# Optimization experiments

Hardware: AMD Instinct MI355X
Metric: run time of the kernel (lower is better)

The kernel has to match this reference:

```python
import jax, jax.numpy as jnp
import numpy as np

HEAD, SIZE = 16, 64
DIM = HEAD * SIZE
NINF = -10000.0
EPS = 1e-6


def setup_inputs() -> dict:
    key = jax.random.key(0)
    ks = jax.random.split(key, 12)
    B, S = 4, 2048
    std = 0.02
    return {
        "x": jax.random.normal(ks[0], (B, S, DIM), jnp.float32),
        "mask": jax.random.randint(ks[1], (B, S), 0, 2, jnp.int32),
        "wq_w": jax.random.normal(ks[2], (DIM, DIM), jnp.float32) * std,
        "wq_b": jnp.zeros((DIM,), jnp.float32),
        "wk_w": jax.random.normal(ks[3], (DIM, DIM), jnp.float32) * std,
        "wk_b": jnp.zeros((DIM,), jnp.float32),
        "wv_w": jax.random.normal(ks[4], (DIM, DIM), jnp.float32) * std,
        "wv_b": jnp.zeros((DIM,), jnp.float32),
        "dense_w": jax.random.normal(ks[5], (DIM, DIM), jnp.float32) * std,
        "dense_b": jnp.zeros((DIM,), jnp.float32),
        "gamma": jnp.ones((DIM,), jnp.float32),
        "beta": jnp.zeros((DIM,), jnp.float32),
    }


def _split_heads(t):
    # [B, S, DIM] -> [B, H, S, size]
    B, S, _ = t.shape
    return t.reshape(B, S, HEAD, SIZE).transpose(0, 2, 1, 3)


def _layernorm(x, gamma, beta):
    mu = jnp.mean(x, axis=-1, keepdims=True)
    var = jnp.mean(jnp.square(x - mu), axis=-1, keepdims=True)
    return (x - mu) * jax.lax.rsqrt(var + EPS) * gamma + beta


def reference(x, mask, wq_w, wq_b, wk_w, wk_b, wv_w, wv_b, dense_w, dense_b, gamma, beta):
    B, S, _ = x.shape
    q = _split_heads(x @ wq_w + wq_b)
    k = _split_heads(x @ wk_w + wk_b)
    v = _split_heads(x @ wv_w + wv_b)
    # scores [B, H, S, S]
    scores = jnp.einsum("bhqd,bhkd->bhqk", q, k) / jnp.sqrt(jnp.float32(SIZE))
    scores = scores + mask.astype(jnp.float32)[:, None, None, :] * NINF
    attn = jax.nn.softmax(scores, axis=-1)
    ctx = jnp.einsum("bhqk,bhkd->bhqd", attn, v)  # [B, H, S, size]
    ctx = ctx.transpose(0, 2, 1, 3).reshape(B, S, DIM)
    out = _layernorm(x + (ctx @ dense_w + dense_b), gamma, beta)
    return out, attn
```

## Files before the change

### kernel.cpp

```cpp
#include <hip/hip_runtime.h>
#include <stdint.h>

#define NB 4
#define NS 2048
#define NH 16
#define HSZ 64
#define ND 1024
#define NM (NB*NS)
#define QSCALE 0.180336880f

typedef unsigned short u16;
typedef unsigned int u32;
typedef __attribute__((ext_vector_type(4))) float f32x4;
typedef __attribute__((ext_vector_type(8))) __bf16 bf16x8;

static __device__ __forceinline__ u16 f2bf(float f){
  unsigned int x = __builtin_bit_cast(unsigned int, f);
  x += 0x7fffu + ((x >> 16) & 1u);
  return (u16)(x >> 16);
}
static __device__ __forceinline__ u16 f2bf_rz(float f){
  return (u16)(__builtin_bit_cast(unsigned int, f) >> 16);
}

#define GLDS16(gp, lp) __builtin_amdgcn_global_load_lds( \
    (const __attribute__((address_space(1))) void*)(gp),  \
    (__attribute__((address_space(3))) void*)(lp), 16, 0, 0)

__global__ __launch_bounds__(256) void k_cast(const float4* __restrict__ in,
                                              ushort4* __restrict__ out, int n4){
  int i = blockIdx.x*256 + threadIdx.x;
  if (i >= n4) return;
  float4 v = in[i];
  ushort4 o;
  o.x = f2bf(v.x); o.y = f2bf(v.y); o.z = f2bf(v.z); o.w = f2bf(v.w);
  out[i] = o;
}

__global__ __launch_bounds__(256) void k_transpose4(const float* __restrict__ wq,
    const float* __restrict__ wk, const float* __restrict__ wv,
    const float* __restrict__ wd, u16* __restrict__ wcat, u16* __restrict__ wdt){
  __shared__ float t[32][33];
  const int z = blockIdx.z;
  const float* in = (z==0) ? wq : (z==1) ? wk : (z==2) ? wv : wd;
  u16* out = (z<3) ? (wcat + (size_t)z*ND*ND) : wdt;
  int tx = threadIdx.x & 31, ty = threadIdx.x >> 5;
  int n0 = blockIdx.x*32, k0 = blockIdx.y*32;
  #pragma unroll
  for (int i=0;i<32;i+=8)
    t[ty+i][tx] = in[(size_t)(k0+ty+i)*ND + n0 + tx];
  __syncthreads();
  #pragma unroll
  for (int i=0;i<32;i+=8)
    out[(size_t)(n0+ty+i)*ND + k0 + tx] = f2bf(t[tx][ty+i]);
}

template<int EPI>
__global__ __launch_bounds__(256,2) void k_gemm(const u16* __restrict__ A,
    const u16* __restrict__ Bt, const float* __restrict__ b0,
    const float* __restrict__ b1, const float* __restrict__ b2,
    const float* __restrict__ resid, u16* __restrict__ Qo, u16* __restrict__ Ko,
    u16* __restrict__ Vto, float* __restrict__ Out){
  __shared__ u16 sA[128*64];
  __shared__ u16 sB[128*64];
  const int tid = threadIdx.x;
  const int wave = tid >> 6, lane = tid & 63;
  const int l15 = lane & 15, l4 = lane >> 4;
  const int m0 = blockIdx.x * 128, n0 = blockIdx.y * 128;
  const int wm = wave >> 1, wn = wave & 1;
  const f32x4 vz = {0.f,0.f,0.f,0.f};
  f32x4 acc[4][4];
  #pragma unroll
  for (int i=0;i<4;i++)
    #pragma unroll
    for (int j=0;j<4;j++) acc[i][j] = vz;

  for (int k0 = 0; k0 < 1024; k0 += 64){
    __syncthreads();
    #pragma unroll
    for (int t=0; t<4; t++){
      const int jb = (t*4 + wave)*64;
      const int j  = jb + lane;
      const int r = j >> 3, c = (j & 7) << 3;
      GLDS16(A  + (((size_t)(m0 + r)) << 10) + (size_t)(k0 + c), sA + jb*8);
      GLDS16(Bt + (((size_t)(n0 + r)) << 10) + (size_t)(k0 + c), sB + jb*8);
    }
    __syncthreads();
    #pragma unroll
    for (int kk=0; kk<64; kk+=32){
      bf16x8 af[4], bv[4];
      #pragma unroll
      for (int mi=0;mi<4;mi++)
        af[mi] = *(const bf16x8*)(const void*)(sA + (wm*64 + mi*16 + l15)*64 + kk + l4*8);
      #pragma unroll
      for (int ni=0;ni<4;ni++)
        bv[ni] = *(const bf16x8*)(const void*)(sB + (wn*64 + ni*16 + l15)*64 + kk + l4*8);
      #pragma unroll
      for (int mi=0;mi<4;mi++)
        #pragma unroll
        for (int ni=0;ni<4;ni++)
          acc[mi][ni] = __builtin_amdgcn_mfma_f32_16x16x32_bf16(af[mi], bv[ni], acc[mi][ni], 0, 0, 0);
    }
  }

  if (EPI == 0){
    const int sec = n0 >> 10;
    const float* bias = (sec==0) ? b0 : (sec==1) ? b1 : b2;
    const float scale = (sec==0) ? QSCALE : 1.0f;
    u16* dst = (sec==0) ? Qo : (sec==1) ? Ko : Vto;
    #pragma unroll
    for (int mi=0;mi<4;mi++){
      #pragma unroll
      for (int ni=0;ni<4;ni++){
        const int n = n0 + wn*64 + ni*16 + l15;
        const int nn = n & (ND-1);
        const int h = nn >> 6, d = nn & 63;
        const float bvv = bias[nn];
        #pragma unroll
        for (int j=0;j<4;j++){
          const int m = m0 + wm*64 + mi*16 + l4*4 + j;
          const int b = m >> 11, s = m & (NS-1);
          const float v = (acc[mi][ni][j] + bvv) * scale;
          if (sec < 2)
            dst[((((size_t)b*NH + h)*NS + s) << 6) + d] = f2bf(v);
          else
            dst[((((size_t)b*NH + h)*HSZ + d) << 11) + s] = f2bf(v);
        }
      }
    }
  } else {
    #pragma unroll
    for (int mi=0;mi<4;mi++){
      #pragma unroll
      for (int ni=0;ni<4;ni++){
        const int n = n0 + wn*64 + ni*16 + l15;
        const float bvv = b0[n];
        #pragma unroll
        for (int j=0;j<4;j++){
          const int m = m0 + wm*64 + mi*16 + l4*4 + j;
          const size_t o = ((size_t)m << 10) + n;
          Out[o] = acc[mi][ni][j] + bvv + resid[o];
        }
      }
    }
  }
}

static __device__ __forceinline__ void attn_decode(int bid, int& qb, int& bh){
  const int x = bid & 7, t = bid >> 3;
  qb = t & 15;
  bh = (t >> 4) * 8 + x;
}

__global__ __launch_bounds__(512,4) void k_attn_stats(const u16* __restrict__ Q,
    const u16* __restrict__ K, const int* __restrict__ mask,
    float* __restrict__ stats){
  __shared__ u16 sK[64][72];
  const int tid = threadIdx.x, wave = tid>>6, lane = tid&63;
  const int l15 = lane&15, l4 = lane>>4;
  int qb, bh; attn_decode(blockIdx.x, qb, bh);
  const int b = bh >> 4;
  const size_t hoff = (size_t)bh * NS * HSZ;
  const int q0 = qb*128 + wave*16;
  const bf16x8 qf0 = *(const bf16x8*)(const void*)(Q + hoff + (size_t)(q0+l15)*HSZ + l4*8);
  const bf16x8 qf1 = *(const bf16x8*)(const void*)(Q + hoff + (size_t)(q0+l15)*HSZ + 32 + l4*8);
  const f32x4 vz = {0.f,0.f,0.f,0.f};
  float lr[4] = {0.f,0.f,0.f,0.f};
  for (int kb=0; kb<NS; kb+=64){
    __syncthreads();
    {
      const int r = tid >> 3, c = (tid & 7) << 3;
      *(int4*)(void*)&sK[r][c] = *(const int4*)(const void*)(K + hoff + (size_t)(kb+r)*HSZ + c);
    }
    __syncthreads();
    #pragma unroll
    for (int n=0;n<4;n++){
      bf16x8 kf0 = *(const bf16x8*)(const void*)&sK[n*16+l15][l4*8];
      bf16x8 kf1 = *(const bf16x8*)(const void*)&sK[n*16+l15][32+l4*8];
      f32x4 a = vz;
      a = __builtin_amdgcn_mfma_f32_16x16x32_bf16(qf0, kf0, a, 0,0,0);
      a = __builtin_amdgcn_mfma_f32_16x16x32_bf16(qf1, kf1, a, 0,0,0);
      const int key = kb + n*16 + l15;
      const bool msk = mask[b*NS + key] != 0;
      #pragma unroll
      for (int j=0;j<4;j++)
        lr[j] += msk ? 0.f : __builtin_amdgcn_exp2f(a[j]);
    }
  }
  #pragma unroll
  for (int j=0;j<4;j++){
    float l = lr[j];
    #pragma unroll
    for (int off=1; off<16; off<<=1)
      l += __shfl_xor(l, off, 64);
    if (l15 == 0)
      stats[(size_t)bh*NS + q0 + l4*4 + j] = 1.f/l;
  }
}

__global__ __launch_bounds__(512,4) void k_attn_pv(const u16* __restrict__ Q,
    const u16* __restrict__ K, const u16* __restrict__ Vt,
    const int* __restrict__ mask, const float* __restrict__ stats,
    float* __restrict__ attn, u16* __restrict__ ctx){
  __shared__ u16 sK[64][72];
  __shared__ u16 sV[64][72];
  __shared__ u16 sP[8][16][72];
  const int tid = threadIdx.x, wave = tid>>6, lane = tid&63;
  const int l15 = lane&15, l4 = lane>>4;
  int qb, bh; attn_decode(blockIdx.x, qb, bh);
  const int b = bh >> 4, h = bh & 15;
  const size_t hoff = (size_t)bh * NS * HSZ;
  const int q0 = qb*128 + wave*16;
  const bf16x8 qf0 = *(const bf16x8*)(const void*)(Q + hoff + (size_t)(q0+l15)*HSZ + l4*8);
  const bf16x8 qf1 = *(const bf16x8*)(const void*)(Q + hoff + (size_t)(q0+l15)*HSZ + 32 + l4*8);
  float rinv[4];
  #pragma unroll
  for (int j=0;j<4;j++)
    rinv[j] = stats[(size_t)bh*NS + q0 + l4*4 + j];
  const f32x4 vz = {0.f,0.f,0.f,0.f};
  f32x4 cacc[4];
  #pragma unroll
  for (int i=0;i<4;i++) cacc[i] = vz;
  float* attn_base = attn + (size_t)bh * NS * NS;

  for (int kb=0; kb<NS; kb+=64){
    __syncthreads();
    {
      const int r = tid >> 3, c = (tid & 7) << 3;
      *(int4*)(void*)&sK[r][c] = *(const int4*)(const void*)(K  + hoff + (size_t)(kb+r)*HSZ + c);
      *(int4*)(void*)&sV[r][c] = *(const int4*)(const void*)(Vt + hoff + (size_t)r*NS + kb + c);
    }
    __syncthreads();
    #pragma unroll
    for (int n=0;n<4;n++){
      bf16x8 kf0 = *(const bf16x8*)(const void*)&sK[n*16+l15][l4*8];
      bf16x8 kf1 = *(const bf16x8*)(const void*)&sK[n*16+l15][32+l4*8];
      f32x4 a = vz;
      a = __builtin_amdgcn_mfma_f32_16x16x32_bf16(qf0, kf0, a, 0,0,0);
      a = __builtin_amdgcn_mfma_f32_16x16x32_bf16(qf1, kf1, a, 0,0,0);
      const int key = kb + n*16 + l15;
      const bool msk = mask[b*NS + key] != 0;
      #pragma unroll
      for (int j=0;j<4;j++){
        const float e = msk ? 0.f : __builtin_amdgcn_exp2f(a[j]);
        sP[wave][l4*4+j][n*16+l15] = f2bf_rz(e * rinv[j]);
      }
    }
    #pragma unroll
    for (int kk=0;kk<2;kk++){
      bf16x8 pf = *(const bf16x8*)(const void*)&sP[wave][l15][kk*32 + l4*8];
      #pragma unroll
      for (int n2=0;n2<4;n2++){
        bf16x8 vf = *(const bf16x8*)(const void*)&sV[n2*16+l15][kk*32 + l4*8];
        cacc[n2] = __builtin_amdgcn_mfma_f32_16x16x32_bf16(pf, vf, cacc[n2], 0,0,0);
      }
    }
    #pragma unroll
    for (int jj=0;jj<4;jj++){
      const int r = jj*4 + l4;
      const uint2 pw = *(const uint2*)(const void*)&sP[wave][r][l15*4];
      f32x4 o;
      o.x = __builtin_bit_cast(float, pw.x << 16);
      o.y = __builtin_bit_cast(float, pw.x & 0xffff0000u);
      o.z = __builtin_bit_cast(float, pw.y << 16);
      o.w = __builtin_bit_cast(float, pw.y & 0xffff0000u);
      __builtin_nontemporal_store(o,
          (f32x4*)(void*)&attn_base[(size_t)(q0 + r)*NS + kb + l15*4]);
    }
  }
  #pragma unroll
  for (int n2=0;n2<4;n2++)
    #pragma unroll
    for (int j=0;j<4;j++){
      const int q = q0 + l4*4 + j;
      ctx[(((size_t)(b*NS + q)) << 10) + h*HSZ + n2*16 + l15] = f2bf(cacc[n2][j]);
    }
}

__global__ __launch_bounds__(256) void k_layernorm(float* __restrict__ buf,
    const float* __restrict__ gamma, const float* __restrict__ beta){
  const int row = blockIdx.x, tid = threadIdx.x;
  float4* rp = (float4*)(buf + ((size_t)row << 10));
  float4 a = rp[tid];
  float s  = a.x + a.y + a.z + a.w;
  float ss = a.x*a.x + a.y*a.y + a.z*a.z + a.w*a.w;
  #pragma unroll
  for (int off=1; off<64; off<<=1){
    s  += __shfl_xor(s,  off, 64);
    ss += __shfl_xor(ss, off, 64);
  }
  __shared__ float red[8];
  const int wave = tid>>6, lane = tid&63;
  if (lane == 0){ red[wave] = s; red[wave+4] = ss; }
  __syncthreads();
  s  = red[0]+red[1]+red[2]+red[3];
  ss = red[4]+red[5]+red[6]+red[7];
  const float mu  = s * (1.f/1024.f);
  const float var = ss * (1.f/1024.f) - mu*mu;
  const float rs  = rsqrtf(var + 1e-6f);
  float4 g  = ((const float4*)gamma)[tid];
  float4 be = ((const float4*)beta)[tid];
  float4 o;
  o.x = (a.x-mu)*rs*g.x + be.x;
  o.y = (a.y-mu)*rs*g.y + be.y;
  o.z = (a.z-mu)*rs*g.z + be.z;
  o.w = (a.w-mu)*rs*g.w + be.w;
  rp[tid] = o;
}

extern "C" void kernel_launch(void* const* d_in, const int* in_sizes, int n_in,
                              void* d_out, int out_size, void* d_ws, size_t ws_size,
                              hipStream_t stream){
  const float* x     = (const float*)d_in[0];
  const int*   mask  = (const int*)d_in[1];
  const float* wq_w  = (const float*)d_in[2];
  const float* wq_b  = (const float*)d_in[3];
  const float* wk_w  = (const float*)d_in[4];
  const float* wk_b  = (const float*)d_in[5];
  const float* wv_w  = (const float*)d_in[6];
  const float* wv_b  = (const float*)d_in[7];
  const float* wd_w  = (const float*)d_in[8];
  const float* wd_b  = (const float*)d_in[9];
  const float* gamma = (const float*)d_in[10];
  const float* beta  = (const float*)d_in[11];

  float* out0 = (float*)d_out;
  float* attn = out0 + (size_t)NM * ND;

  char* ws = (char*)d_ws;
  u16*   xb    = (u16*)(ws);
  u16*   ctx   = (u16*)(ws);
  u16*   wcat  = (u16*)(ws + (16u<<20));
  u16*   wdt   = (u16*)(ws + (22u<<20));
  u16*   Qb    = (u16*)(ws + (24u<<20));
  u16*   Kb    = (u16*)(ws + (40u<<20));
  u16*   Vtb   = (u16*)(ws + (56u<<20));
  float* stats = (float*)(ws + (72u<<20));

  k_cast<<<8192, 256, 0, stream>>>((const float4*)x, (ushort4*)xb, NM*ND/4);
  k_transpose4<<<dim3(32,32,4), 256, 0, stream>>>(wq_w, wk_w, wv_w, wd_w, wcat, wdt);

  k_gemm<0><<<dim3(64,24), 256, 0, stream>>>(xb, wcat, wq_b, wk_b, wv_b,
                                             nullptr, Qb, Kb, Vtb, nullptr);

  k_attn_stats<<<1024, 512, 0, stream>>>(Qb, Kb, mask, stats);
  k_attn_pv<<<1024, 512, 0, stream>>>(Qb, Kb, Vtb, mask, stats, attn, ctx);

  k_gemm<2><<<dim3(64,8), 256, 0, stream>>>(ctx, wdt, wd_b, nullptr, nullptr,
                                            x, nullptr, nullptr, nullptr, out0);
  k_layernorm<<<NM, 256, 0, stream>>>(out0, gamma, beta);
}
```

Before: 454.2 us.

## Double-buffer K/V shared-memory tiles with register prefetch in attention kernels

Both attention kernels now keep two shared-memory buffers for the K (and V) tiles and prefetch the next-next tile into registers while computing on the current one. This cuts the two barriers per iteration down to one and is meant to hide global load latency behind the MFMA and exp work. It doubles K/V LDS usage and holds extra registers live, which could lower occupancy. The attention kernel is likely bound by writing the large fp32 attn output, so the benefit may be limited.

```diff
diff --git a/kernel.cpp b/kernel.cpp
--- a/kernel.cpp
+++ b/kernel.cpp
@@ -155,28 +155,35 @@
 __global__ __launch_bounds__(512,4) void k_attn_stats(const u16* __restrict__ Q,
     const u16* __restrict__ K, const int* __restrict__ mask,
     float* __restrict__ stats){
-  __shared__ u16 sK[64][72];
+  __shared__ u16 sK[2][64][72];
   const int tid = threadIdx.x, wave = tid>>6, lane = tid&63;
   const int l15 = lane&15, l4 = lane>>4;
   int qb, bh; attn_decode(blockIdx.x, qb, bh);
   const int b = bh >> 4;
   const size_t hoff = (size_t)bh * NS * HSZ;
   const int q0 = qb*128 + wave*16;
+  const u16* Kg = K + hoff;
   const bf16x8 qf0 = *(const bf16x8*)(const void*)(Q + hoff + (size_t)(q0+l15)*HSZ + l4*8);
   const bf16x8 qf1 = *(const bf16x8*)(const void*)(Q + hoff + (size_t)(q0+l15)*HSZ + 32 + l4*8);
   const f32x4 vz = {0.f,0.f,0.f,0.f};
+  const int r = tid >> 3, c = (tid & 7) << 3;
   float lr[4] = {0.f,0.f,0.f,0.f};
+
+  int4 rK = *(const int4*)(const void*)(Kg + (size_t)r*HSZ + c);
+  *(int4*)(void*)&sK[0][r][c] = rK;
+  rK = *(const int4*)(const void*)(Kg + (size_t)(64+r)*HSZ + c);
+  __syncthreads();
+
   for (int kb=0; kb<NS; kb+=64){
-    __syncthreads();
-    {
-      const int r = tid >> 3, c = (tid & 7) << 3;
-      *(int4*)(void*)&sK[r][c] = *(const int4*)(const void*)(K + hoff + (size_t)(kb+r)*HSZ + c);
-    }
-    __syncthreads();
+    const int cur = (kb>>6)&1;
+    if (kb+64 < NS)
+      *(int4*)(void*)&sK[cur^1][r][c] = rK;
+    if (kb+128 < NS)
+      rK = *(const int4*)(const void*)(Kg + (size_t)(kb+128+r)*HSZ + c);
     #pragma unroll
     for (int n=0;n<4;n++){
-      bf16x8 kf0 = *(const bf16x8*)(const void*)&sK[n*16+l15][l4*8];
-      bf16x8 kf1 = *(const bf16x8*)(const void*)&sK[n*16+l15][32+l4*8];
+      bf16x8 kf0 = *(const bf16x8*)(const void*)&sK[cur][n*16+l15][l4*8];
+      bf16x8 kf1 = *(const bf16x8*)(const void*)&sK[cur][n*16+l15][32+l4*8];
       f32x4 a = vz;
       a = __builtin_amdgcn_mfma_f32_16x16x32_bf16(qf0, kf0, a, 0,0,0);
       a = __builtin_amdgcn_mfma_f32_16x16x32_bf16(qf1, kf1, a, 0,0,0);
@@ -186,6 +193,7 @@
       for (int j=0;j<4;j++)
         lr[j] += msk ? 0.f : __builtin_amdgcn_exp2f(a[j]);
     }
+    __syncthreads();
   }
   #pragma unroll
   for (int j=0;j<4;j++){
@@ -202,8 +210,8 @@
     const u16* __restrict__ K, const u16* __restrict__ Vt,
     const int* __restrict__ mask, const float* __restrict__ stats,
     float* __restrict__ attn, u16* __restrict__ ctx){
-  __shared__ u16 sK[64][72];
-  __shared__ u16 sV[64][72];
+  __shared__ u16 sK[2][64][72];
+  __shared__ u16 sV[2][64][72];
   __shared__ u16 sP[8][16][72];
   const int tid = threadIdx.x, wave = tid>>6, lane = tid&63;
   const int l15 = lane&15, l4 = lane>>4;
@@ -211,6 +219,8 @@
   const int b = bh >> 4, h = bh & 15;
   const size_t hoff = (size_t)bh * NS * HSZ;
   const int q0 = qb*128 + wave*16;
+  const u16* Kg = K + hoff;
+  const u16* Vg = Vt + hoff;
   const bf16x8 qf0 = *(const bf16x8*)(const void*)(Q + hoff + (size_t)(q0+l15)*HSZ + l4*8);
   const bf16x8 qf1 = *(const bf16x8*)(const void*)(Q + hoff + (size_t)(q0+l15)*HSZ + 32 + l4*8);
   float rinv[4];
@@ -222,19 +232,30 @@
   #pragma unroll
   for (int i=0;i<4;i++) cacc[i] = vz;
   float* attn_base = attn + (size_t)bh * NS * NS;
+  const int r = tid >> 3, c = (tid & 7) << 3;
+
+  int4 rK = *(const int4*)(const void*)(Kg + (size_t)r*HSZ + c);
+  int4 rV = *(const int4*)(const void*)(Vg + (size_t)r*NS + c);
+  *(int4*)(void*)&sK[0][r][c] = rK;
+  *(int4*)(void*)&sV[0][r][c] = rV;
+  rK = *(const int4*)(const void*)(Kg + (size_t)(64+r)*HSZ + c);
+  rV = *(const int4*)(const void*)(Vg + (size_t)r*NS + 64 + c);
+  __syncthreads();
 
   for (int kb=0; kb<NS; kb+=64){
-    __syncthreads();
-    {
-      const int r = tid >> 3, c = (tid & 7) << 3;
-      *(int4*)(void*)&sK[r][c] = *(const int4*)(const void*)(K  + hoff + (size_t)(kb+r)*HSZ + c);
-      *(int4*)(void*)&sV[r][c] = *(const int4*)(const void*)(Vt + hoff + (size_t)r*NS + kb + c);
-    }
-    __syncthreads();
+    const int cur = (kb>>6)&1;
+    if (kb+64 < NS){
+      *(int4*)(void*)&sK[cur^1][r][c] = rK;
+      *(int4*)(void*)&sV[cur^1][r][c] = rV;
+    }
+    if (kb+128 < NS){
+      rK = *(const int4*)(const void*)(Kg + (size_t)(kb+128+r)*HSZ + c);
+      rV = *(const int4*)(const void*)(Vg + (size_t)r*NS + (kb+128) + c);
+    }
     #pragma unroll
     for (int n=0;n<4;n++){
-      bf16x8 kf0 = *(const bf16x8*)(const void*)&sK[n*16+l15][l4*8];
-      bf16x8 kf1 = *(const bf16x8*)(const void*)&sK[n*16+l15][32+l4*8];
+      bf16x8 kf0 = *(const bf16x8*)(const void*)&sK[cur][n*16+l15][l4*8];
+      bf16x8 kf1 = *(const bf16x8*)(const void*)&sK[cur][n*16+l15][32+l4*8];
       f32x4 a = vz;
       a = __builtin_amdgcn_mfma_f32_16x16x32_bf16(qf0, kf0, a, 0,0,0);
       a = __builtin_amdgcn_mfma_f32_16x16x32_bf16(qf1, kf1, a, 0,0,0);
@@ -251,22 +272,23 @@
       bf16x8 pf = *(const bf16x8*)(const void*)&sP[wave][l15][kk*32 + l4*8];
       #pragma unroll
       for (int n2=0;n2<4;n2++){
-        bf16x8 vf = *(const bf16x8*)(const void*)&sV[n2*16+l15][kk*32 + l4*8];
+        bf16x8 vf = *(const bf16x8*)(const void*)&sV[cur][n2*16+l15][kk*32 + l4*8];
         cacc[n2] = __builtin_amdgcn_mfma_f32_16x16x32_bf16(pf, vf, cacc[n2], 0,0,0);
       }
     }
     #pragma unroll
     for (int jj=0;jj<4;jj++){
-      const int r = jj*4 + l4;
-      const uint2 pw = *(const uint2*)(const void*)&sP[wave][r][l15*4];
+      const int rr = jj*4 + l4;
+      const uint2 pw = *(const uint2*)(const void*)&sP[wave][rr][l15*4];
       f32x4 o;
       o.x = __builtin_bit_cast(float, pw.x << 16);
       o.y = __builtin_bit_cast(float, pw.x & 0xffff0000u);
       o.z = __builtin_bit_cast(float, pw.y << 16);
       o.w = __builtin_bit_cast(float, pw.y & 0xffff0000u);
       __builtin_nontemporal_store(o,
-          (f32x4*)(void*)&attn_base[(size_t)(q0 + r)*NS + kb + l15*4]);
-    }
+          (f32x4*)(void*)&attn_base[(size_t)(q0 + rr)*NS + kb + l15*4]);
+    }
+    __syncthreads();
   }
   #pragma unroll
   for (int n2=0;n2<4;n2++)
```

After: 415.2 us. 1.09x faster.
